# Optimization experiments

Hardware: AMD Instinct MI355X
Metric: run time of the kernel (lower is better)

## Reference

```python
import jax, jax.numpy as jnp
import numpy as np

N_NODES = 20000
N_EDGES = 640000
D = 128          # vision_dim == topo_dim
OUT = 256        # out_dim
B = 64           # image batch == num graphs
HW = 64
NEG_SLOPE = 0.2


def _sn(w2d, u):
    """PyTorch spectral_norm forward: one power iteration (u,v detached), W/sigma."""
    v = jax.lax.stop_gradient(w2d.T @ u)
    v = v / (jnp.linalg.norm(v) + 1e-12)
    u2 = jax.lax.stop_gradient(w2d @ v)
    u2 = u2 / (jnp.linalg.norm(u2) + 1e-12)
    sigma = u2 @ (w2d @ v)
    return w2d / sigma


def _leaky(x):
    return jnp.where(x >= 0, x, NEG_SLOPE * x)


def setup_inputs() -> dict:
    key = jax.random.key(0)
    ks = jax.random.split(key, 16)
    vis = jax.random.normal(ks[0], (B, D, HW, HW), dtype=jnp.float32)
    topo = jax.random.normal(ks[1], (N_NODES, D), dtype=jnp.float32)
    edge_index = jax.random.randint(ks[2], (2, N_EDGES), 0, N_NODES, dtype=jnp.int64)
    batch = jnp.sort(jax.random.randint(ks[3], (N_NODES,), 0, B, dtype=jnp.int64))
    s = 0.05
    conv_w = jax.random.normal(ks[4], (D, D, 3, 3), dtype=jnp.float32) * s
    conv_b = jnp.zeros((D,), dtype=jnp.float32)
    conv_u = jax.random.normal(ks[5], (D,), dtype=jnp.float32)
    fcv_w = jax.random.normal(ks[6], (OUT, D * 4), dtype=jnp.float32) * s
    fcv_b = jnp.zeros((OUT,), dtype=jnp.float32)
    fcv_u = jax.random.normal(ks[7], (OUT,), dtype=jnp.float32)
    gcn_w = jax.random.normal(ks[8], (D, D), dtype=jnp.float32) * s
    gcn_b = jnp.zeros((D,), dtype=jnp.float32)
    fct_w = jax.random.normal(ks[9], (OUT, D), dtype=jnp.float32) * s
    fct_b = jnp.zeros((OUT,), dtype=jnp.float32)
    fct_u = jax.random.normal(ks[10], (OUT,), dtype=jnp.float32)
    return dict(vis=vis, topo=topo, edge_index=edge_index, batch=batch,
                conv_w=conv_w, conv_b=conv_b, conv_u=conv_u,
                fcv_w=fcv_w, fcv_b=fcv_b, fcv_u=fcv_u,
                gcn_w=gcn_w, gcn_b=gcn_b,
                fct_w=fct_w, fct_b=fct_b, fct_u=fct_u)


def reference(vis, topo, edge_index, batch,
              conv_w, conv_b, conv_u,
              fcv_w, fcv_b, fcv_u,
              gcn_w, gcn_b,
              fct_w, fct_b, fct_u):
    # ---- vision head: spectral-norm conv3x3 -> leaky_relu -> adaptive max pool 2x2 -> SN linear
    cw = _sn(conv_w.reshape(D, -1), conv_u).reshape(conv_w.shape)
    x = jax.lax.conv_general_dilated(vis, cw, window_strides=(1, 1), padding='VALID',
                                     dimension_numbers=('NCHW', 'OIHW', 'NCHW'))
    x = _leaky(x + conv_b[None, :, None, None])              # [B, D, 62, 62]
    Bc, C, H, W = x.shape
    x = x.reshape(Bc, C, 2, H // 2, 2, W // 2).max(axis=(3, 5))  # adaptive max pool -> [B,D,2,2]
    x = x.reshape(Bc, -1)                                    # [B, 4D]
    vis_score = x @ _sn(fcv_w, fcv_u).T + fcv_b              # [B, OUT]

    # ---- topo head: GCNConv (sym-norm, self-loops) -> leaky_relu -> global max pool -> SN linear
    n = topo.shape[0]
    loop = jnp.arange(n, dtype=edge_index.dtype)
    src = jnp.concatenate([edge_index[0], loop])
    dst = jnp.concatenate([edge_index[1], loop])
    deg = jax.ops.segment_sum(jnp.ones_like(dst, dtype=topo.dtype), dst, num_segments=n)
    dis = jnp.where(deg > 0, jax.lax.rsqrt(jnp.maximum(deg, 1.0)), 0.0)
    norm = dis[src] * dis[dst]                               # [E+N]
    xw = topo @ gcn_w                                        # [N, D]
    h = jax.ops.segment_sum(norm[:, None] * xw[src], dst, num_segments=n) + gcn_b
    h = _leaky(h)
    pooled = jax.ops.segment_max(h, batch, num_segments=B)   # [B, D]
    topo_score = pooled @ _sn(fct_w, fct_u).T + fct_b        # [B, OUT]

    return (vis_score, topo_score)
```

## Files before the change

### kernel.cpp

```cpp
#include <hip/hip_runtime.h>
#include <hip/hip_bf16.h>
#include <float.h>
#include <stdint.h>

#define NB   64
#define CD   128
#define OUTD 256
#define NNODE 20000
#define NEDGE 640000

typedef __bf16 bf16x8 __attribute__((ext_vector_type(8)));
typedef __bf16 bf16x4 __attribute__((ext_vector_type(4)));
typedef float  f32x4  __attribute__((ext_vector_type(4)));

__device__ inline void gl_lds16(const void* g, void* l) {
  __builtin_amdgcn_global_load_lds(
      (const __attribute__((address_space(1))) void*)g,
      (__attribute__((address_space(3))) void*)l, 16, 0, 0);
}

__device__ inline void atomicMaxF(float* addr, float val) {
  if (val >= 0.f) atomicMax((int*)addr, __float_as_int(val));
  else            atomicMin((unsigned int*)addr, __float_as_uint(val));
}

__global__ void k_init(float* __restrict__ pooled_v, float* __restrict__ pooled_t,
                       int* __restrict__ cnt, int* __restrict__ fill,
                       float* __restrict__ sn_scratch, int* __restrict__ ntotal) {
  const int i = blockIdx.x * 256 + threadIdx.x;
  if (i < NB * CD * 4) pooled_v[i] = -FLT_MAX;
  if (i < NB * CD)     pooled_t[i] = -FLT_MAX;
  if (i < NNODE)       { cnt[i] = 0; fill[i] = 0; }
  if (i < 1796)        sn_scratch[i] = 0.0f;
  if (i == 0)          *ntotal = 0;
}

__global__ __launch_bounds__(256) void k_sn_v(const float* __restrict__ conv_w, const float* __restrict__ conv_u,
                                              const float* __restrict__ fcv_w,  const float* __restrict__ fcv_u,
                                              const float* __restrict__ fct_w,  const float* __restrict__ fct_u,
                                              float* __restrict__ sn) {
  const int bb = blockIdx.x;
  const float* W; const float* u; float* v; int C; int r0;
  if (bb < 16)      { W = conv_w; u = conv_u; v = sn;        C = 1152; r0 = bb * 8; }
  else if (bb < 48) { W = fcv_w;  u = fcv_u;  v = sn + 1152; C = 512;  r0 = (bb - 16) * 8; }
  else              { W = fct_w;  u = fct_u;  v = sn + 1664; C = 128;  r0 = (bb - 48) * 8; }
  const int tid = threadIdx.x;
  float acc[5] = {0.f, 0.f, 0.f, 0.f, 0.f};
  for (int i = r0; i < r0 + 8; ++i) {
    const float ui = u[i];
    const float* row = W + (size_t)i * C;
    #pragma unroll
    for (int t = 0; t < 5; ++t) {
      const int j = tid + t * 256;
      if (j < C) acc[t] += ui * row[j];
    }
  }
  #pragma unroll
  for (int t = 0; t < 5; ++t) {
    const int j = tid + t * 256;
    if (j < C) atomicAdd(&v[j], acc[t]);
  }
}

__global__ __launch_bounds__(256) void k_sn_w(const float* __restrict__ conv_w,
                                              const float* __restrict__ fcv_w,
                                              const float* __restrict__ fct_w,
                                              float* __restrict__ sn) {
  const int gw = blockIdx.x * 4 + (threadIdx.x >> 6);
  const int lane = threadIdx.x & 63;
  const float* W; const float* v; int C, m, row;
  if (gw < 128)      { W = conv_w; v = sn;        C = 1152; m = 0; row = gw; }
  else if (gw < 384) { W = fcv_w;  v = sn + 1152; C = 512;  m = 1; row = gw - 128; }
  else               { W = fct_w;  v = sn + 1664; C = 128;  m = 2; row = gw - 384; }
  const float* wr = W + (size_t)row * C;
  float y = 0.f;
  for (int c = lane; c < C; c += 64) y += wr[c] * v[c];
  #pragma unroll
  for (int s = 32; s > 0; s >>= 1) y += __shfl_xor(y, s, 64);
  if (lane == 0) atomicAdd(&sn[1792 + m], y * y);
}

__global__ __launch_bounds__(256) void k_sn_fin(const float* __restrict__ sn, float* __restrict__ inv_sigma) {
  __shared__ float red[256];
  const int tid = threadIdx.x;
  const int off[4] = {0, 1152, 1664, 1792};
  for (int m = 0; m < 3; ++m) {
    const int C = off[m + 1] - off[m];
    float ss = 0.f;
    for (int j = tid; j < C; j += 256) { const float a = sn[off[m] + j]; ss += a * a; }
    red[tid] = ss; __syncthreads();
    for (int s = 128; s > 0; s >>= 1) { if (tid < s) red[tid] += red[tid + s]; __syncthreads(); }
    if (tid == 0) inv_sigma[m] = (sqrtf(red[0]) + 1e-12f) / sqrtf(sn[1792 + m]);
    __syncthreads();
  }
}

__global__ __launch_bounds__(256) void k_prep(const float* __restrict__ vis, __hip_bfloat16* __restrict__ visT2,
                                              const float* __restrict__ conv_w, const float* __restrict__ inv_sigma,
                                              __hip_bfloat16* __restrict__ Bt2,
                                              const int* __restrict__ dst, int* __restrict__ cnt) {
  __shared__ float tile[8192];
  const int bid = blockIdx.x;
  const int t = threadIdx.x;
  if (bid < 4096) {
    const int b = bid >> 6, y = bid & 63;
    const int c0 = t >> 4, x4 = (t & 15) << 2;
    const float* src = vis + (size_t)b * 524288 + y * 64;
    #pragma unroll
    for (int i = 0; i < 8; ++i) {
      const int c = i * 16 + c0;
      *(f32x4*)&tile[c * 64 + x4] = *(const f32x4*)(src + (size_t)c * 4096 + x4);
    }
    __syncthreads();
    bf16x8* dstv = (bf16x8*)(visT2 + ((size_t)bid << 13));
    #pragma unroll
    for (int k = 0; k < 4; ++k) {
      const int j = k * 256 + t;
      const int g = j >> 6, x = j & 63;
      union { bf16x8 v; __hip_bfloat16 h[8]; } u;
      #pragma unroll
      for (int cc = 0; cc < 8; ++cc)
        u.h[cc] = __float2bfloat16(tile[(g * 8 + cc) * 64 + x]);
      dstv[j] = u.v;
    }
  } else if (bid < 4672) {
    const int tt = (bid - 4096) * 256 + t;
    if (tt < 147456) {
      const int j = tt & 7, n = (tt >> 3) & 127, s = (tt >> 10) & 7, hk = (tt >> 13) & 1, tap = tt >> 14;
      const int ci = hk * 64 + s * 8 + j;
      Bt2[tt] = __float2bfloat16(conv_w[n * 1152 + ci * 9 + tap] * inv_sigma[0]);
    }
  } else {
    const int e = (bid - 4672) * 256 + t;
    if (e < NEDGE) atomicAdd(&cnt[dst[e]], 1);
  }
}

__global__ __launch_bounds__(256, 4) void k_conv(const __hip_bfloat16* __restrict__ visT2,
                                                 const __hip_bfloat16* __restrict__ Bt2,
                                                 const float* __restrict__ conv_b,
                                                 float* __restrict__ pooled_v) {
  __shared__ bf16x8 lds_a[1024];
  __shared__ bf16x8 lds_b[1024];
  const int bx = blockIdx.x;
  const int b = bx / 31;
  const int y0 = (bx - b * 31) * 2;
  const int tid = threadIdx.x;
  const int wave = tid >> 6, lane = tid & 63;
  const int quad = lane >> 4, l15 = lane & 15;

  f32x4 acc[8][2];
  #pragma unroll
  for (int i = 0; i < 8; ++i) {
    acc[i][0] = f32x4{0.f, 0.f, 0.f, 0.f};
    acc[i][1] = f32x4{0.f, 0.f, 0.f, 0.f};
  }

  const __hip_bfloat16* vb = visT2 + ((size_t)b << 19);
  const int s0 = wave << 1;
  bf16x8* ldsA0 = &lds_a[s0 << 7];
  bf16x8* ldsB0 = &lds_b[s0 << 7];
  const int lane8 = lane << 3;

  for (int ky = 0; ky < 3; ++ky) {
    for (int kx = 0; kx < 3; ++kx) {
      const int tap = ky * 3 + kx;
      #pragma unroll
      for (int hk = 0; hk < 2; ++hk) {
        const __hip_bfloat16* a0p = vb + ((size_t)(((y0 + ky) << 4) + (hk << 3) + s0) << 9) + (kx << 3) + lane8;
        const __hip_bfloat16* a1p = vb + ((size_t)(((y0 + 1 + ky) << 4) + (hk << 3) + s0) << 9) + (kx << 3) + lane8;
        const __hip_bfloat16* bp  = Bt2 + (((size_t)(((tap << 1) + hk) << 3) + s0) << 10) + lane8;
        gl_lds16(a0p,        ldsA0);
        gl_lds16(a1p,        ldsA0 + 64);
        gl_lds16(a0p + 512,  ldsA0 + 128);
        gl_lds16(a1p + 512,  ldsA0 + 192);
        gl_lds16(bp,         ldsB0);
        gl_lds16(bp + 512,   ldsB0 + 64);
        gl_lds16(bp + 1024,  ldsB0 + 128);
        gl_lds16(bp + 1536,  ldsB0 + 192);
        __syncthreads();
        const bf16x8 b00 = lds_b[(quad << 7) + (wave << 5) + l15];
        const bf16x8 b01 = lds_b[(quad << 7) + (wave << 5) + 16 + l15];
        const bf16x8 b10 = lds_b[((4 + quad) << 7) + (wave << 5) + l15];
        const bf16x8 b11 = lds_b[((4 + quad) << 7) + (wave << 5) + 16 + l15];
        #pragma unroll
        for (int mt = 0; mt < 8; ++mt) {
          const bf16x8 a0 = lds_a[(quad << 7) + (mt << 4) + l15];
          const bf16x8 a1 = lds_a[((4 + quad) << 7) + (mt << 4) + l15];
          acc[mt][0] = __builtin_amdgcn_mfma_f32_16x16x32_bf16(a0, b00, acc[mt][0], 0, 0, 0);
          acc[mt][1] = __builtin_amdgcn_mfma_f32_16x16x32_bf16(a0, b01, acc[mt][1], 0, 0, 0);
          acc[mt][0] = __builtin_amdgcn_mfma_f32_16x16x32_bf16(a1, b10, acc[mt][0], 0, 0, 0);
          acc[mt][1] = __builtin_amdgcn_mfma_f32_16x16x32_bf16(a1, b11, acc[mt][1], 0, 0, 0);
        }
        __syncthreads();
      }
    }
  }

  const float cb0 = conv_b[(wave << 5) + l15];
  const float cb1 = conv_b[(wave << 5) + 16 + l15];
  float pmax[2][2][2];
  #pragma unroll
  for (int i = 0; i < 8; ++i) (&pmax[0][0][0])[i] = -FLT_MAX;

  #pragma unroll
  for (int mt = 0; mt < 8; ++mt) {
    const int py = (y0 + (mt >> 2)) >= 31 ? 1 : 0;
    #pragma unroll
    for (int r = 0; r < 4; ++r) {
      const int x = ((mt & 3) << 4) + (quad << 2) + r;
      if (x < 62) {
        const int px = x >= 31 ? 1 : 0;
        float v0 = acc[mt][0][r] + cb0;  v0 = v0 >= 0.f ? v0 : 0.2f * v0;
        float v1 = acc[mt][1][r] + cb1;  v1 = v1 >= 0.f ? v1 : 0.2f * v1;
        pmax[0][py][px] = fmaxf(pmax[0][py][px], v0);
        pmax[1][py][px] = fmaxf(pmax[1][py][px], v1);
      }
    }
  }
  #pragma unroll
  for (int nt = 0; nt < 2; ++nt)
    #pragma unroll
    for (int py = 0; py < 2; ++py)
      #pragma unroll
      for (int px = 0; px < 2; ++px) {
        float v = pmax[nt][py][px];
        v = fmaxf(v, __shfl_xor(v, 16, 64));
        v = fmaxf(v, __shfl_xor(v, 32, 64));
        if (quad == 0) {
          const int n = (wave << 5) + (nt << 4) + l15;
          atomicMaxF(&pooled_v[(size_t)b * 512 + n * 4 + py * 2 + px], v);
        }
      }
}

__global__ __launch_bounds__(256) void k_scan_xw(const int* __restrict__ cnt, int* __restrict__ offset,
                                                 int* __restrict__ total, float* __restrict__ dis,
                                                 const float* __restrict__ topo, const float* __restrict__ gcn_w,
                                                 __bf16* __restrict__ xws) {
  __shared__ f32x4 w4[4096];
  __shared__ int sbase;
  const int tid = threadIdx.x;
  if (blockIdx.x < 79) {
    int* red = (int*)w4;
    const int n = blockIdx.x * 256 + tid;
    const int v = (n < NNODE) ? cnt[n] : 0;
    red[tid] = v; __syncthreads();
    for (int d = 1; d < 256; d <<= 1) {
      const int t = (tid >= d) ? red[tid - d] : 0;
      __syncthreads();
      red[tid] += t;
      __syncthreads();
    }
    if (tid == 255) sbase = atomicAdd(total, red[255]);
    __syncthreads();
    if (n < NNODE) {
      offset[n] = sbase + red[tid] - v;
      dis[n] = rsqrtf((float)(v + 1));
    }
  } else {
    const f32x4* gw4 = (const f32x4*)gcn_w;
    for (int i = tid; i < 4096; i += 256) w4[i] = gw4[i];
    __syncthreads();
    const int n0 = (blockIdx.x - 79) * 64;
    const int jq = tid & 31, ns = tid >> 5;
    for (int pass = 0; pass < 8; ++pass) {
      const int n = n0 + pass * 8 + ns;
      if (n >= NNODE) break;
      const f32x4* tr4 = (const f32x4*)(topo + (size_t)n * 128);
      f32x4 a = {0.f, 0.f, 0.f, 0.f};
      for (int d4 = 0; d4 < 32; ++d4) {
        const f32x4 t = tr4[d4];
        const int base = (d4 << 7) + jq;
        #pragma unroll
        for (int m = 0; m < 4; ++m) {
          const f32x4 w = w4[base + m * 32];
          #pragma unroll
          for (int k = 0; k < 4; ++k) a[k] += t[m] * w[k];
        }
      }
      const float dn = rsqrtf((float)(cnt[n] + 1));
      bf16x4 o;
      #pragma unroll
      for (int k = 0; k < 4; ++k) o[k] = (__bf16)(a[k] * dn);
      ((bf16x4*)xws)[(size_t)n * 32 + jq] = o;
    }
  }
}

__global__ void k_bucket(const int* __restrict__ src, const int* __restrict__ dst,
                         const int* __restrict__ offset, int* __restrict__ fill,
                         int* __restrict__ sorted_src) {
  const int e = blockIdx.x * 256 + threadIdx.x;
  if (e >= NEDGE) return;
  const int t = dst[e];
  const int pos = atomicAdd(&fill[t], 1);
  sorted_src[offset[t] + pos] = src[e];
}

__global__ __launch_bounds__(256) void k_gather(const int* __restrict__ sorted_src,
                                                const int* __restrict__ offset, const int* __restrict__ cnt,
                                                const float* __restrict__ dis, const __bf16* __restrict__ xws,
                                                const float* __restrict__ gcn_b, __bf16* __restrict__ h) {
  const int wave = threadIdx.x >> 6, lane = threadIdx.x & 63;
  const int n = blockIdx.x * 4 + wave;
  const int slot = lane >> 4, l16 = lane & 15;
  const int e0 = offset[n], ne = cnt[n];
  const bf16x8* x8 = (const bf16x8*)xws;
  float a[8];
  if (slot == 0) {
    const bf16x8 v = x8[(size_t)n * 16 + l16];
    #pragma unroll
    for (int k = 0; k < 8; ++k) a[k] = (float)v[k];
  } else {
    #pragma unroll
    for (int k = 0; k < 8; ++k) a[k] = 0.f;
  }
  for (int e = slot; e < ne; e += 4) {
    const int s = sorted_src[e0 + e];
    const bf16x8 v = x8[(size_t)s * 16 + l16];
    #pragma unroll
    for (int k = 0; k < 8; ++k) a[k] += (float)v[k];
  }
  #pragma unroll
  for (int k = 0; k < 8; ++k) {
    a[k] += __shfl_xor(a[k], 16, 64);
    a[k] += __shfl_xor(a[k], 32, 64);
  }
  if (slot == 0) {
    const float dn = dis[n];
    bf16x8 o;
    #pragma unroll
    for (int k = 0; k < 8; ++k) {
      float t = gcn_b[(l16 << 3) + k] + dn * a[k];
      t = t >= 0.f ? t : 0.2f * t;
      o[k] = (__bf16)t;
    }
    ((bf16x8*)h)[(size_t)n * 16 + l16] = o;
  }
}

__global__ void k_pool_t(const __bf16* __restrict__ h, const int* __restrict__ batch,
                         float* __restrict__ pooled_t) {
  const int d = threadIdx.x;
  const int n0 = blockIdx.x * 32;
  float run = -FLT_MAX;
  int cur = batch[n0];
  for (int i = 0; i < 32; ++i) {
    const int n = n0 + i;
    const int g = batch[n];
    if (g != cur) {
      atomicMaxF(&pooled_t[cur * 128 + d], run);
      run = -FLT_MAX; cur = g;
    }
    run = fmaxf(run, (float)h[(size_t)n * 128 + d]);
  }
  atomicMaxF(&pooled_t[cur * 128 + d], run);
}

__global__ __launch_bounds__(256) void k_fc(const float* __restrict__ pooled_v, const float* __restrict__ fcv_w,
                                            const float* __restrict__ fcv_b,
                                            const float* __restrict__ pooled_t, const float* __restrict__ fct_w,
                                            const float* __restrict__ fct_b,
                                            const float* __restrict__ inv_sigma, float* __restrict__ out) {
  const int tid = threadIdx.x;
  if (blockIdx.x < 64) {
    __shared__ f32x4 xr[128];
    const int b = blockIdx.x;
    if (tid < 128) xr[tid] = ((const f32x4*)pooled_v)[b * 128 + tid];
    __syncthreads();
    const f32x4* wr = (const f32x4*)(fcv_w + (size_t)tid * 512);
    f32x4 a4 = {0.f, 0.f, 0.f, 0.f};
    for (int f = 0; f < 128; ++f) {
      const f32x4 x = xr[f];
      const f32x4 w = wr[f];
      #pragma unroll
      for (int k = 0; k < 4; ++k) a4[k] += x[k] * w[k];
    }
    const float a = a4[0] + a4[1] + a4[2] + a4[3];
    out[b * 256 + tid] = a * inv_sigma[1] + fcv_b[tid];
  } else {
    __shared__ f32x4 xr2[32];
    const int b = blockIdx.x - 64;
    if (tid < 32) xr2[tid] = ((const f32x4*)pooled_t)[b * 32 + tid];
    __syncthreads();
    const f32x4* wr = (const f32x4*)(fct_w + (size_t)tid * 128);
    f32x4 a4 = {0.f, 0.f, 0.f, 0.f};
    for (int f = 0; f < 32; ++f) {
      const f32x4 x = xr2[f];
      const f32x4 w = wr[f];
      #pragma unroll
      for (int k = 0; k < 4; ++k) a4[k] += x[k] * w[k];
    }
    const float a = a4[0] + a4[1] + a4[2] + a4[3];
    out[NB * 256 + b * 256 + tid] = a * inv_sigma[2] + fct_b[tid];
  }
}

extern "C" void kernel_launch(void* const* d_in, const int* in_sizes, int n_in,
                              void* d_out, int out_size, void* d_ws, size_t ws_size,
                              hipStream_t stream) {
  const float* vis    = (const float*)d_in[0];
  const float* topo   = (const float*)d_in[1];
  const int*   eidx   = (const int*)d_in[2];
  const int*   batch  = (const int*)d_in[3];
  const float* conv_w = (const float*)d_in[4];
  const float* conv_b = (const float*)d_in[5];
  const float* conv_u = (const float*)d_in[6];
  const float* fcv_w  = (const float*)d_in[7];
  const float* fcv_b  = (const float*)d_in[8];
  const float* fcv_u  = (const float*)d_in[9];
  const float* gcn_w  = (const float*)d_in[10];
  const float* gcn_b  = (const float*)d_in[11];
  const float* fct_w  = (const float*)d_in[12];
  const float* fct_b  = (const float*)d_in[13];
  const float* fct_u  = (const float*)d_in[14];
  float* out = (float*)d_out;

  char* p = (char*)d_ws;
  float* inv_sigma  = (float*)p; p += 256;
  float* sn_scratch = (float*)p; p += 1796 * 4 + 240;
  float* pooled_v   = (float*)p; p += (size_t)NB * 512 * 4;
  float* pooled_t   = (float*)p; p += (size_t)NB * 128 * 4;
  int*   cnt        = (int*)p;   p += (size_t)NNODE * 4;
  int*   offset     = (int*)p;   p += (size_t)NNODE * 4;
  int*   fill       = (int*)p;   p += (size_t)NNODE * 4;
  float* dis        = (float*)p; p += (size_t)NNODE * 4;
  int*   ntotal     = (int*)p;   p += 256;
  int*   sorted_src = (int*)p;   p += (size_t)NEDGE * 4;
  __bf16* xws       = (__bf16*)p; p += (size_t)NNODE * 128 * 2 + 256;
  __bf16* h         = (__bf16*)p; p += (size_t)NNODE * 128 * 2 + 256;
  __hip_bfloat16* Bt2 = (__hip_bfloat16*)p; p += (size_t)147456 * 2;
  p = (char*)(((uintptr_t)p + 255) & ~(uintptr_t)255);
  __hip_bfloat16* visT2 = (__hip_bfloat16*)p;

  hipLaunchKernelGGL(k_init,    dim3(128),  dim3(256), 0, stream, pooled_v, pooled_t, cnt, fill, sn_scratch, ntotal);
  hipLaunchKernelGGL(k_sn_v,    dim3(80),   dim3(256), 0, stream, conv_w, conv_u, fcv_w, fcv_u, fct_w, fct_u, sn_scratch);
  hipLaunchKernelGGL(k_sn_w,    dim3(160),  dim3(256), 0, stream, conv_w, fcv_w, fct_w, sn_scratch);
  hipLaunchKernelGGL(k_sn_fin,  dim3(1),    dim3(256), 0, stream, sn_scratch, inv_sigma);
  hipLaunchKernelGGL(k_prep,    dim3(7172), dim3(256), 0, stream, vis, visT2, conv_w, inv_sigma, Bt2, eidx + NEDGE, cnt);
  hipLaunchKernelGGL(k_conv,    dim3(64*31), dim3(256), 0, stream, visT2, Bt2, conv_b, pooled_v);
  hipLaunchKernelGGL(k_scan_xw, dim3(392),  dim3(256), 0, stream, cnt, offset, ntotal, dis, topo, gcn_w, xws);
  hipLaunchKernelGGL(k_bucket,  dim3(2500), dim3(256), 0, stream, eidx, eidx + NEDGE, offset, fill, sorted_src);
  hipLaunchKernelGGL(k_gather,  dim3(5000), dim3(256), 0, stream, sorted_src, offset, cnt, dis, xws, gcn_b, h);
  hipLaunchKernelGGL(k_pool_t,  dim3(625),  dim3(128), 0, stream, h, batch, pooled_t);
  hipLaunchKernelGGL(k_fc,      dim3(128),  dim3(256), 0, stream, pooled_v, fcv_w, fcv_b, pooled_t, fct_w, fct_b, inv_sigma, out);
}
```

Measured before the change: 489.0 us.

## Fuse topo max-pool into GCN gather and split conv launch in halves

```diff
diff --git a/kernel.cpp b/kernel.cpp
--- a/kernel.cpp
+++ b/kernel.cpp
@@ -139,12 +139,12 @@
 __global__ __launch_bounds__(256, 4) void k_conv(const __hip_bfloat16* __restrict__ visT2,
                                                  const __hip_bfloat16* __restrict__ Bt2,
                                                  const float* __restrict__ conv_b,
-                                                 float* __restrict__ pooled_v) {
+                                                 float* __restrict__ pooled_v, int b0) {
   __shared__ bf16x8 lds_a[1024];
   __shared__ bf16x8 lds_b[1024];
   const int bx = blockIdx.x;
-  const int b = bx / 31;
-  const int y0 = (bx - b * 31) * 2;
+  const int b = b0 + bx / 31;
+  const int y0 = (bx % 31) * 2;
   const int tid = threadIdx.x;
   const int wave = tid >> 6, lane = tid & 63;
   const int quad = lane >> 4, l15 = lane & 15;
@@ -301,7 +301,10 @@
 __global__ __launch_bounds__(256) void k_gather(const int* __restrict__ sorted_src,
                                                 const int* __restrict__ offset, const int* __restrict__ cnt,
                                                 const float* __restrict__ dis, const __bf16* __restrict__ xws,
-                                                const float* __restrict__ gcn_b, __bf16* __restrict__ h) {
+                                                const float* __restrict__ gcn_b, const int* __restrict__ batch,
+                                                float* __restrict__ pooled_t) {
+  __shared__ float hred[4][128];
+  __shared__ int hg[4];
   const int wave = threadIdx.x >> 6, lane = threadIdx.x & 63;
   const int n = blockIdx.x * 4 + wave;
   const int slot = lane >> 4, l16 = lane & 15;
@@ -327,35 +330,29 @@
     a[k] += __shfl_xor(a[k], 16, 64);
     a[k] += __shfl_xor(a[k], 32, 64);
   }
+  if (lane == 0) hg[wave] = batch[n];
   if (slot == 0) {
     const float dn = dis[n];
-    bf16x8 o;
     #pragma unroll
     for (int k = 0; k < 8; ++k) {
       float t = gcn_b[(l16 << 3) + k] + dn * a[k];
-      t = t >= 0.f ? t : 0.2f * t;
-      o[k] = (__bf16)t;
-    }
-    ((bf16x8*)h)[(size_t)n * 16 + l16] = o;
-  }
-}
-
-__global__ void k_pool_t(const __bf16* __restrict__ h, const int* __restrict__ batch,
-                         float* __restrict__ pooled_t) {
-  const int d = threadIdx.x;
-  const int n0 = blockIdx.x * 32;
-  float run = -FLT_MAX;
-  int cur = batch[n0];
-  for (int i = 0; i < 32; ++i) {
-    const int n = n0 + i;
-    const int g = batch[n];
-    if (g != cur) {
-      atomicMaxF(&pooled_t[cur * 128 + d], run);
-      run = -FLT_MAX; cur = g;
-    }
-    run = fmaxf(run, (float)h[(size_t)n * 128 + d]);
-  }
-  atomicMaxF(&pooled_t[cur * 128 + d], run);
+      hred[wave][(l16 << 3) + k] = t >= 0.f ? t : 0.2f * t;
+    }
+  }
+  __syncthreads();
+  const int tid = threadIdx.x;
+  if (tid < 128) {
+    const int g0 = hg[0], g1 = hg[1], g2 = hg[2], g3 = hg[3];
+    if (g0 == g1 && g1 == g2 && g2 == g3) {
+      const float m = fmaxf(fmaxf(hred[0][tid], hred[1][tid]), fmaxf(hred[2][tid], hred[3][tid]));
+      atomicMaxF(&pooled_t[g0 * 128 + tid], m);
+    } else {
+      atomicMaxF(&pooled_t[g0 * 128 + tid], hred[0][tid]);
+      atomicMaxF(&pooled_t[g1 * 128 + tid], hred[1][tid]);
+      atomicMaxF(&pooled_t[g2 * 128 + tid], hred[2][tid]);
+      atomicMaxF(&pooled_t[g3 * 128 + tid], hred[3][tid]);
+    }
+  }
 }
 
 __global__ __launch_bounds__(256) void k_fc(const float* __restrict__ pooled_v, const float* __restrict__ fcv_w,
@@ -429,7 +426,6 @@
   int*   ntotal     = (int*)p;   p += 256;
   int*   sorted_src = (int*)p;   p += (size_t)NEDGE * 4;
   __bf16* xws       = (__bf16*)p; p += (size_t)NNODE * 128 * 2 + 256;
-  __bf16* h         = (__bf16*)p; p += (size_t)NNODE * 128 * 2 + 256;
   __hip_bfloat16* Bt2 = (__hip_bfloat16*)p; p += (size_t)147456 * 2;
   p = (char*)(((uintptr_t)p + 255) & ~(uintptr_t)255);
   __hip_bfloat16* visT2 = (__hip_bfloat16*)p;
@@ -439,10 +435,10 @@
   hipLaunchKernelGGL(k_sn_w,    dim3(160),  dim3(256), 0, stream, conv_w, fcv_w, fct_w, sn_scratch);
   hipLaunchKernelGGL(k_sn_fin,  dim3(1),    dim3(256), 0, stream, sn_scratch, inv_sigma);
   hipLaunchKernelGGL(k_prep,    dim3(7172), dim3(256), 0, stream, vis, visT2, conv_w, inv_sigma, Bt2, eidx + NEDGE, cnt);
-  hipLaunchKernelGGL(k_conv,    dim3(64*31), dim3(256), 0, stream, visT2, Bt2, conv_b, pooled_v);
+  hipLaunchKernelGGL(k_conv,    dim3(32*31), dim3(256), 0, stream, visT2, Bt2, conv_b, pooled_v, 0);
+  hipLaunchKernelGGL(k_conv,    dim3(32*31), dim3(256), 0, stream, visT2, Bt2, conv_b, pooled_v, 32);
   hipLaunchKernelGGL(k_scan_xw, dim3(392),  dim3(256), 0, stream, cnt, offset, ntotal, dis, topo, gcn_w, xws);
   hipLaunchKernelGGL(k_bucket,  dim3(2500), dim3(256), 0, stream, eidx, eidx + NEDGE, offset, fill, sorted_src);
-  hipLaunchKernelGGL(k_gather,  dim3(5000), dim3(256), 0, stream, sorted_src, offset, cnt, dis, xws, gcn_b, h);
-  hipLaunchKernelGGL(k_pool_t,  dim3(625),  dim3(128), 0, stream, h, batch, pooled_t);
+  hipLaunchKernelGGL(k_gather,  dim3(5000), dim3(256), 0, stream, sorted_src, offset, cnt, dis, xws, gcn_b, batch, pooled_t);
   hipLaunchKernelGGL(k_fc,      dim3(128),  dim3(256), 0, stream, pooled_v, fcv_w, fcv_b, pooled_t, fct_w, fct_b, inv_sigma, out);
 }
```

New measurement: 487.2 us. No clear change (-0.4%).
